# Performance work log

Measured on AMD Instinct MI355X. Metric: run time of the kernel, lower is better.

## Reference

```python
import jax, jax.numpy as jnp
import numpy as np

N_MESH, N_GRID, N_EDGES, D, H = 40962, 200000, 600000, 128, 128


def layer_norm(x, g, b, eps=1e-5):
    mu = x.mean(-1, keepdims=True)
    xc = x - mu
    var = (xc * xc).mean(-1, keepdims=True)
    return xc * jax.lax.rsqrt(var + eps) * g + b


def setup_inputs() -> dict:
    key = jax.random.key(0)
    ks = jax.random.split(key, 16)
    s = 1.0 / np.sqrt(D).astype(np.float32)
    s2 = 1.0 / np.sqrt(2 * D).astype(np.float32)
    return {
        "m2g_efeat": jax.random.normal(ks[0], (N_EDGES, D), jnp.float32),
        "grid_nfeat": jax.random.normal(ks[1], (N_GRID, D), jnp.float32),
        "mesh_nfeat": jax.random.normal(ks[2], (N_MESH, D), jnp.float32),
        "src_idx": jax.random.randint(ks[3], (N_EDGES,), 0, N_MESH, jnp.int32),
        "dst_idx": jnp.sort(jax.random.randint(ks[4], (N_EDGES,), 0, N_GRID, jnp.int32)),
        # edge TMLP (first linear split across efeat/src/dst -- equals Linear on concat)
        "We": jax.random.normal(ks[5], (D, H), jnp.float32) * s,
        "Ws": jax.random.normal(ks[6], (D, H), jnp.float32) * s,
        "Wd": jax.random.normal(ks[7], (D, H), jnp.float32) * s,
        "b0": jnp.zeros((H,), jnp.float32),
        "W1e": jax.random.normal(ks[8], (H, D), jnp.float32) * s,
        "b1e": jnp.zeros((D,), jnp.float32),
        "ge": jnp.ones((D,), jnp.float32),
        "be": jnp.zeros((D,), jnp.float32),
        # node MLP: input = concat(grid_nfeat, aggregated_efeat) -> 2D
        "Wn0": jax.random.normal(ks[9], (2 * D, H), jnp.float32) * s2,
        "bn0": jnp.zeros((H,), jnp.float32),
        "Wn1": jax.random.normal(ks[10], (H, D), jnp.float32) * s,
        "bn1": jnp.zeros((D,), jnp.float32),
        "gn": jnp.ones((D,), jnp.float32),
        "bn": jnp.zeros((D,), jnp.float32),
    }


def reference(m2g_efeat, grid_nfeat, mesh_nfeat, src_idx, dst_idx,
              We, Ws, Wd, b0, W1e, b1e, ge, be,
              Wn0, bn0, Wn1, bn1, gn, bn):
    # edge TMLP: project each input tensor then gather (CUGO truncated-MLP form)
    h = jax.nn.silu(m2g_efeat @ We
                    + (mesh_nfeat @ Ws)[src_idx]
                    + (grid_nfeat @ Wd)[dst_idx]
                    + b0)                                  # [E, H]
    efeat = layer_norm(h @ W1e + b1e, ge, be)              # [E, D]
    # sum aggregation edge->node, then concat with dst node features
    agg = jax.ops.segment_sum(efeat, dst_idx, num_segments=grid_nfeat.shape[0])  # [N_grid, D]
    cat = jnp.concatenate([grid_nfeat, agg], axis=-1)      # [N_grid, 2D]
    hn = jax.nn.silu(cat @ Wn0 + bn0)                      # [N_grid, H]
    dst = layer_norm(hn @ Wn1 + bn1, gn, bn) + grid_nfeat  # residual
    return dst
```

## Files before the change

### kernel.cpp

```cpp
#include <hip/hip_runtime.h>
#include <math.h>

#define NM 40962
#define NG 200000
#define NE 600000

typedef unsigned short u16;
typedef unsigned int u32;
typedef __attribute__((ext_vector_type(8))) short short8;
typedef __attribute__((ext_vector_type(4))) float f32x4;

#define OFF_WE 0
#define OFF_WS 16384
#define OFF_WD 32768
#define OFF_W1 49152
#define OFF_W0 65536
#define OFF_WN1 98304
__device__ u16 g_wp[114688];

__device__ __forceinline__ u32 f2bf(float f) {
  u32 u = __float_as_uint(f);
  return (u + 0x7FFFu + ((u >> 16) & 1u)) >> 16;
}
__device__ __forceinline__ float bfl(u32 h) { return __uint_as_float(h << 16); }
__device__ __forceinline__ float bsel(u32 w, int hiHalf) {
  return hiHalf ? __uint_as_float(w & 0xFFFF0000u) : __uint_as_float(w << 16);
}
__device__ __forceinline__ float silu_f(float x) { return x / (1.f + __expf(-x)); }

#define MFMA16(a, b, c) __builtin_amdgcn_mfma_f32_16x16x32_bf16(a, b, c, 0, 0, 0)

__device__ __forceinline__ void pk8(const float4& a, const float4& b, short8& hi,
                                    short8& lo) {
  float f[8] = {a.x, a.y, a.z, a.w, b.x, b.y, b.z, b.w};
#pragma unroll
  for (int j = 0; j < 8; ++j) {
    u32 h = f2bf(f[j]);
    hi[j] = (short)h;
    lo[j] = (short)f2bf(f[j] - bfl(h));
  }
}

__device__ __forceinline__ void afrag_hl(const float* __restrict__ X, int row, int k0,
                                         short8& hi, short8& lo) {
  const float4* p = (const float4*)(X + (size_t)row * 128 + k0);
  pk8(p[0], p[1], hi, lo);
}

template <int K>
__device__ __forceinline__ short8 bfrag(const u16* __restrict__ Wp, int n, int k0) {
  return *(const short8*)(Wp + (size_t)n * K + k0);
}

__global__ void prep_all(const float* __restrict__ We, const float* __restrict__ Ws,
                         const float* __restrict__ Wd, const float* __restrict__ W1e,
                         const float* __restrict__ Wn0, const float* __restrict__ Wn1) {
  for (int i = blockIdx.x * blockDim.x + threadIdx.x; i < 114688;
       i += gridDim.x * blockDim.x) {
    const float* W;
    int loc, kb;
    if (i < 16384)       { W = We;  loc = i;         kb = 7; }
    else if (i < 32768)  { W = Ws;  loc = i - 16384; kb = 7; }
    else if (i < 49152)  { W = Wd;  loc = i - 32768; kb = 7; }
    else if (i < 65536)  { W = W1e; loc = i - 49152; kb = 7; }
    else if (i < 98304)  { W = Wn0; loc = i - 65536; kb = 8; }
    else                 { W = Wn1; loc = i - 98304; kb = 7; }
    int n = loc >> kb, k = loc & ((1 << kb) - 1);
    g_wp[i] = (u16)f2bf(W[(size_t)k * 128 + n]);
  }
}

__global__ __launch_bounds__(256) void proj_kernel(const float* __restrict__ mesh,
                                                   const float* __restrict__ gridf,
                                                   uint4* __restrict__ PS,
                                                   uint4* __restrict__ PD,
                                                   float* __restrict__ agg) {
  const int TM = (NM + 31) / 32;
  const int TG = NG / 32;
  const int lane = threadIdx.x & 63, wv = threadIdx.x >> 6;
  const int g = lane >> 4, c = lane & 15;
  const int nw = gridDim.x * 4;
  for (int t = blockIdx.x * 4 + wv; t < TM + TG; t += nw) {
    const float* X;
    const u16* Wp;
    uint4* O;
    int n0, nrows, zero;
    if (t < TM) { X = mesh;  Wp = g_wp + OFF_WS; O = PS; n0 = t * 32;        nrows = NM; zero = 0; }
    else        { X = gridf; Wp = g_wp + OFF_WD; O = PD; n0 = (t - TM) * 32; nrows = NG; zero = 1; }
    f32x4 acc[2][8];
#pragma unroll
    for (int mt = 0; mt < 2; ++mt)
#pragma unroll
      for (int nt = 0; nt < 8; ++nt) {
        f32x4 z = {0.f, 0.f, 0.f, 0.f};
        acc[mt][nt] = z;
      }
#pragma unroll
    for (int kt = 0; kt < 4; ++kt) {
      short8 ah[2], al[2];
#pragma unroll
      for (int mt = 0; mt < 2; ++mt) {
        int row = n0 + 16 * mt + c;
        if (row >= nrows) row = nrows - 1;
        afrag_hl(X, row, 32 * kt + 8 * g, ah[mt], al[mt]);
      }
#pragma unroll
      for (int nt = 0; nt < 8; ++nt) {
        short8 b = bfrag<128>(Wp, 16 * nt + c, 32 * kt + 8 * g);
#pragma unroll
        for (int mt = 0; mt < 2; ++mt) {
          acc[mt][nt] = MFMA16(ah[mt], b, acc[mt][nt]);
          acc[mt][nt] = MFMA16(al[mt], b, acc[mt][nt]);
        }
      }
    }
#pragma unroll
    for (int mt = 0; mt < 2; ++mt)
#pragma unroll
      for (int r = 0; r < 4; ++r) {
        int row = n0 + 16 * mt + 4 * g + r;
        if (row < nrows) {
          uint4 v;
          v.x = f2bf(acc[mt][0][r]) | (f2bf(acc[mt][1][r]) << 16);
          v.y = f2bf(acc[mt][2][r]) | (f2bf(acc[mt][3][r]) << 16);
          v.z = f2bf(acc[mt][4][r]) | (f2bf(acc[mt][5][r]) << 16);
          v.w = f2bf(acc[mt][6][r]) | (f2bf(acc[mt][7][r]) << 16);
          O[(size_t)row * 16 + c] = v;
          if (zero) {
            float4 z = {0.f, 0.f, 0.f, 0.f};
            float4* ap = (float4*)(agg + (size_t)row * 128 + c * 8);
            ap[0] = z;
            ap[1] = z;
          }
        }
      }
  }
}

__global__ __launch_bounds__(256) void edge_kernel(
    const float* __restrict__ m2g, const uint4* __restrict__ PS,
    const uint4* __restrict__ PD, const int* __restrict__ src_idx,
    const int* __restrict__ dst_idx, const float* __restrict__ b0,
    const float* __restrict__ b1e, const float* __restrict__ ge,
    const float* __restrict__ be, float* __restrict__ agg) {
  const u16* WpE = g_wp + OFF_WE;
  const u16* Wp1 = g_wp + OFF_W1;
  __shared__ __align__(16) u16 hbh[4][32][128];
  __shared__ __align__(16) u16 hbl[4][32][128];
  const int lane = threadIdx.x & 63, wv = threadIdx.x >> 6;
  const int g = lane >> 4, c = lane & 15;
  float b0p[8];
#pragma unroll
  for (int nt = 0; nt < 8; ++nt) b0p[nt] = b0[16 * nt + c];
  const int nw = gridDim.x * 4;
  for (int t = blockIdx.x * 4 + wv; t < NE / 32; t += nw) {
    const int e0 = t * 32;
    float4 av[2][4][2];
#pragma unroll
    for (int mt = 0; mt < 2; ++mt)
#pragma unroll
      for (int kt = 0; kt < 4; ++kt) {
        const float4* p =
            (const float4*)(m2g + (size_t)(e0 + 16 * mt + c) * 128 + 32 * kt + 8 * g);
        av[mt][kt][0] = p[0];
        av[mt][kt][1] = p[1];
      }
    int dd[2][4];
    uint4 ps[2][4], pd[2][4];
#pragma unroll
    for (int mt = 0; mt < 2; ++mt)
#pragma unroll
      for (int r = 0; r < 4; ++r) {
        int e = e0 + 16 * mt + 4 * g + r;
        int s = src_idx[e];
        int d = dst_idx[e];
        dd[mt][r] = d;
        ps[mt][r] = PS[(size_t)s * 16 + c];
        pd[mt][r] = PD[(size_t)d * 16 + c];
      }
    f32x4 acc[2][8];
#pragma unroll
    for (int mt = 0; mt < 2; ++mt)
#pragma unroll
      for (int nt = 0; nt < 8; ++nt) {
        f32x4 z = {0.f, 0.f, 0.f, 0.f};
        acc[mt][nt] = z;
      }
#pragma unroll
    for (int kt = 0; kt < 4; ++kt) {
      short8 ah[2], al[2];
#pragma unroll
      for (int mt = 0; mt < 2; ++mt) pk8(av[mt][kt][0], av[mt][kt][1], ah[mt], al[mt]);
#pragma unroll
      for (int nt = 0; nt < 8; ++nt) {
        short8 b = bfrag<128>(WpE, 16 * nt + c, 32 * kt + 8 * g);
#pragma unroll
        for (int mt = 0; mt < 2; ++mt) {
          acc[mt][nt] = MFMA16(ah[mt], b, acc[mt][nt]);
          acc[mt][nt] = MFMA16(al[mt], b, acc[mt][nt]);
        }
      }
    }
#pragma unroll
    for (int mt = 0; mt < 2; ++mt)
#pragma unroll
      for (int nt = 0; nt < 8; ++nt)
#pragma unroll
        for (int r = 0; r < 4; ++r) {
          u32 pw = ((const u32*)&ps[mt][r])[nt >> 1];
          u32 qw = ((const u32*)&pd[mt][r])[nt >> 1];
          acc[mt][nt][r] += b0p[nt] + bsel(pw, nt & 1) + bsel(qw, nt & 1);
        }
#pragma unroll
    for (int mt = 0; mt < 2; ++mt)
#pragma unroll
      for (int r = 0; r < 4; ++r) {
        int row = 16 * mt + 4 * g + r;
        int sw = (row & 7) << 3;
#pragma unroll
        for (int nt = 0; nt < 8; ++nt) {
          float h = silu_f(acc[mt][nt][r]);
          u32 hb = f2bf(h);
          u32 lb = f2bf(h - bfl(hb));
          int idx = (16 * nt + c) ^ sw;
          hbh[wv][row][idx] = (u16)hb;
          hbl[wv][row][idx] = (u16)lb;
        }
      }
    f32x4 acc2[2][8];
    {
      float b1p[8];
#pragma unroll
      for (int nt = 0; nt < 8; ++nt) b1p[nt] = b1e[16 * nt + c];
#pragma unroll
      for (int mt = 0; mt < 2; ++mt)
#pragma unroll
        for (int nt = 0; nt < 8; ++nt) {
          f32x4 a = {b1p[nt], b1p[nt], b1p[nt], b1p[nt]};
          acc2[mt][nt] = a;
        }
    }
#pragma unroll
    for (int kt = 0; kt < 4; ++kt) {
      short8 ah[2], al[2];
#pragma unroll
      for (int mt = 0; mt < 2; ++mt) {
        int row = 16 * mt + c;
        int idx = (32 * kt + 8 * g) ^ ((c & 7) << 3);
        ah[mt] = *(const short8*)&hbh[wv][row][idx];
        al[mt] = *(const short8*)&hbl[wv][row][idx];
      }
#pragma unroll
      for (int nt = 0; nt < 8; ++nt) {
        short8 b = bfrag<128>(Wp1, 16 * nt + c, 32 * kt + 8 * g);
#pragma unroll
        for (int mt = 0; mt < 2; ++mt) {
          acc2[mt][nt] = MFMA16(ah[mt], b, acc2[mt][nt]);
          acc2[mt][nt] = MFMA16(al[mt], b, acc2[mt][nt]);
        }
      }
    }
    float gep[8], bep[8];
#pragma unroll
    for (int nt = 0; nt < 8; ++nt) {
      gep[nt] = ge[16 * nt + c];
      bep[nt] = be[16 * nt + c];
    }
#pragma unroll
    for (int mt = 0; mt < 2; ++mt) {
#pragma unroll
      for (int r = 0; r < 4; ++r) {
        float sm = 0.f, sq = 0.f;
#pragma unroll
        for (int nt = 0; nt < 8; ++nt) {
          float v = acc2[mt][nt][r];
          sm += v;
          sq += v * v;
        }
#pragma unroll
        for (int m = 1; m < 16; m <<= 1) {
          sm += __shfl_xor(sm, m, 64);
          sq += __shfl_xor(sq, m, 64);
        }
        float mu = sm * (1.f / 128.f);
        float var = sq * (1.f / 128.f) - mu * mu;
        float rs = rsqrtf(var + 1e-5f);
#pragma unroll
        for (int nt = 0; nt < 8; ++nt)
          acc2[mt][nt][r] = (acc2[mt][nt][r] - mu) * rs * gep[nt] + bep[nt];
      }
#pragma unroll
      for (int nt = 0; nt < 8; ++nt) {
        float a = acc2[mt][nt][0];
        int dp = dd[mt][0];
#pragma unroll
        for (int r = 1; r < 4; ++r) {
          if (dd[mt][r] == dp) {
            a += acc2[mt][nt][r];
          } else {
            atomicAdd(agg + (size_t)dp * 128 + 16 * nt + c, a);
            a = acc2[mt][nt][r];
            dp = dd[mt][r];
          }
        }
        atomicAdd(agg + (size_t)dp * 128 + 16 * nt + c, a);
      }
    }
  }
}

__global__ __launch_bounds__(256) void node_kernel(
    const float* __restrict__ gridf, const float* __restrict__ agg,
    const float* __restrict__ bn0, const float* __restrict__ bn1,
    const float* __restrict__ gn, const float* __restrict__ bnv,
    float* __restrict__ out) {
  const u16* Wp0 = g_wp + OFF_W0;
  const u16* Wp1 = g_wp + OFF_WN1;
  __shared__ __align__(16) u16 nbuf[4][32][128];
  const int lane = threadIdx.x & 63, wv = threadIdx.x >> 6;
  const int g = lane >> 4, c = lane & 15;
  float b0p[8], b1p[8];
#pragma unroll
  for (int nt = 0; nt < 8; ++nt) {
    b0p[nt] = bn0[16 * nt + c];
    b1p[nt] = bn1[16 * nt + c];
  }
  const int nw = gridDim.x * 4;
  for (int t = blockIdx.x * 4 + wv; t < NG / 32; t += nw) {
    const int n0 = t * 32;
    f32x4 acc[2][8];
#pragma unroll
    for (int mt = 0; mt < 2; ++mt)
#pragma unroll
      for (int nt = 0; nt < 8; ++nt) {
        f32x4 a = {b0p[nt], b0p[nt], b0p[nt], b0p[nt]};
        acc[mt][nt] = a;
      }
#pragma unroll
    for (int kt = 0; kt < 8; ++kt) {
      const float* src = (kt < 4) ? gridf : agg;
      int k0 = (kt & 3) * 32 + 8 * g;
      short8 ah[2], al[2];
#pragma unroll
      for (int mt = 0; mt < 2; ++mt) afrag_hl(src, n0 + 16 * mt + c, k0, ah[mt], al[mt]);
#pragma unroll
      for (int nt = 0; nt < 8; ++nt) {
        short8 b = bfrag<256>(Wp0, 16 * nt + c, 32 * kt + 8 * g);
#pragma unroll
        for (int mt = 0; mt < 2; ++mt) {
          acc[mt][nt] = MFMA16(ah[mt], b, acc[mt][nt]);
          acc[mt][nt] = MFMA16(al[mt], b, acc[mt][nt]);
        }
      }
    }
#pragma unroll
    for (int mt = 0; mt < 2; ++mt)
#pragma unroll
      for (int r = 0; r < 4; ++r) {
        int row = 16 * mt + 4 * g + r;
        int sw = (row & 7) << 3;
#pragma unroll
        for (int nt = 0; nt < 8; ++nt)
          nbuf[wv][row][(16 * nt + c) ^ sw] = (u16)f2bf(silu_f(acc[mt][nt][r]));
      }
    f32x4 acc2[2][8];
#pragma unroll
    for (int mt = 0; mt < 2; ++mt)
#pragma unroll
      for (int nt = 0; nt < 8; ++nt) {
        f32x4 a = {b1p[nt], b1p[nt], b1p[nt], b1p[nt]};
        acc2[mt][nt] = a;
      }
#pragma unroll
    for (int kt = 0; kt < 4; ++kt) {
      short8 ah[2];
#pragma unroll
      for (int mt = 0; mt < 2; ++mt) {
        int row = 16 * mt + c;
        ah[mt] = *(const short8*)&nbuf[wv][row][(32 * kt + 8 * g) ^ ((c & 7) << 3)];
      }
#pragma unroll
      for (int nt = 0; nt < 8; ++nt) {
        short8 b = bfrag<128>(Wp1, 16 * nt + c, 32 * kt + 8 * g);
#pragma unroll
        for (int mt = 0; mt < 2; ++mt) acc2[mt][nt] = MFMA16(ah[mt], b, acc2[mt][nt]);
      }
    }
    float gp[8], bp[8];
#pragma unroll
    for (int nt = 0; nt < 8; ++nt) {
      gp[nt] = gn[16 * nt + c];
      bp[nt] = bnv[16 * nt + c];
    }
#pragma unroll
    for (int mt = 0; mt < 2; ++mt)
#pragma unroll
      for (int r = 0; r < 4; ++r) {
        float sm = 0.f, sq = 0.f;
#pragma unroll
        for (int nt = 0; nt < 8; ++nt) {
          float v = acc2[mt][nt][r];
          sm += v;
          sq += v * v;
        }
#pragma unroll
        for (int m = 1; m < 16; m <<= 1) {
          sm += __shfl_xor(sm, m, 64);
          sq += __shfl_xor(sq, m, 64);
        }
        float mu = sm * (1.f / 128.f);
        float var = sq * (1.f / 128.f) - mu * mu;
        float rs = rsqrtf(var + 1e-5f);
        int row = n0 + 16 * mt + 4 * g + r;
#pragma unroll
        for (int nt = 0; nt < 8; ++nt) {
          size_t o = (size_t)row * 128 + 16 * nt + c;
          out[o] = (acc2[mt][nt][r] - mu) * rs * gp[nt] + bp[nt] + gridf[o];
        }
      }
  }
}

extern "C" void kernel_launch(void* const* d_in, const int* in_sizes, int n_in,
                              void* d_out, int out_size, void* d_ws, size_t ws_size,
                              hipStream_t stream) {
  const float* m2g = (const float*)d_in[0];
  const float* grid = (const float*)d_in[1];
  const float* mesh = (const float*)d_in[2];
  const int* src = (const int*)d_in[3];
  const int* dst = (const int*)d_in[4];
  const float* We = (const float*)d_in[5];
  const float* Ws = (const float*)d_in[6];
  const float* Wd = (const float*)d_in[7];
  const float* b0 = (const float*)d_in[8];
  const float* W1e = (const float*)d_in[9];
  const float* b1e = (const float*)d_in[10];
  const float* ge = (const float*)d_in[11];
  const float* be = (const float*)d_in[12];
  const float* Wn0 = (const float*)d_in[13];
  const float* bn0 = (const float*)d_in[14];
  const float* Wn1 = (const float*)d_in[15];
  const float* bn1 = (const float*)d_in[16];
  const float* gn = (const float*)d_in[17];
  const float* bnv = (const float*)d_in[18];
  (void)in_sizes; (void)n_in; (void)out_size; (void)ws_size;

  char* ws = (char*)d_ws;
  float* agg = (float*)ws;
  size_t aggB = (size_t)NG * 128 * 4;
  size_t psB = (size_t)NM * 256;
  uint4* PS = (uint4*)(ws + aggB);
  uint4* PD = (uint4*)(ws + aggB + psB);

  prep_all<<<224, 256, 0, stream>>>(We, Ws, Wd, W1e, Wn0, Wn1);
  proj_kernel<<<1024, 256, 0, stream>>>(mesh, grid, PS, PD, agg);
  edge_kernel<<<1536, 256, 0, stream>>>(m2g, PS, PD, src, dst, b0, b1e, ge, be, agg);
  node_kernel<<<1536, 256, 0, stream>>>(grid, agg, bn0, bn1, gn, bnv, (float*)d_out);
}
```

Baseline: 1.210 ms.

## Prefetch next tile's activations into registers across proj, edge and node kernels

Each persistent-wave loop now loads the A-operand rows for the next tile into registers right after the first GEMM's MFMAs, so the global loads overlap with the epilogue and second GEMM instead of stalling at the start of each iteration. The same software-pipelining pattern is applied to the projection, edge and node kernels. It costs extra VGPRs (64 in proj/edge, 128 floats in node), which may reduce occupancy or cause spills.

Measured after the change: 1.249 ms. 3.2% more time.

```diff
diff --git a/kernel.cpp b/kernel.cpp
--- a/kernel.cpp
+++ b/kernel.cpp
@@ -39,12 +39,6 @@
     hi[j] = (short)h;
     lo[j] = (short)f2bf(f[j] - bfl(h));
   }
-}
-
-__device__ __forceinline__ void afrag_hl(const float* __restrict__ X, int row, int k0,
-                                         short8& hi, short8& lo) {
-  const float4* p = (const float4*)(X + (size_t)row * 128 + k0);
-  pk8(p[0], p[1], hi, lo);
 }
 
 template <int K>
@@ -70,6 +64,13 @@
   }
 }
 
+__device__ __forceinline__ void proj_src(int t, const float* mesh, const float* gridf,
+                                         const float*& X, int& n0, int& nrows) {
+  const int TM = (NM + 31) / 32;
+  if (t < TM) { X = mesh;  n0 = t * 32;        nrows = NM; }
+  else        { X = gridf; n0 = (t - TM) * 32; nrows = NG; }
+}
+
 __global__ __launch_bounds__(256) void proj_kernel(const float* __restrict__ mesh,
                                                    const float* __restrict__ gridf,
                                                    uint4* __restrict__ PS,
@@ -77,16 +78,33 @@
                                                    float* __restrict__ agg) {
   const int TM = (NM + 31) / 32;
   const int TG = NG / 32;
+  const int T = TM + TG;
   const int lane = threadIdx.x & 63, wv = threadIdx.x >> 6;
   const int g = lane >> 4, c = lane & 15;
   const int nw = gridDim.x * 4;
-  for (int t = blockIdx.x * 4 + wv; t < TM + TG; t += nw) {
-    const float* X;
-    const u16* Wp;
-    uint4* O;
-    int n0, nrows, zero;
-    if (t < TM) { X = mesh;  Wp = g_wp + OFF_WS; O = PS; n0 = t * 32;        nrows = NM; zero = 0; }
-    else        { X = gridf; Wp = g_wp + OFF_WD; O = PD; n0 = (t - TM) * 32; nrows = NG; zero = 1; }
+  int t0 = blockIdx.x * 4 + wv;
+  if (t0 >= T) return;
+  float4 av[2][4][2];
+  {
+    const float* X; int n0, nrows;
+    proj_src(t0, mesh, gridf, X, n0, nrows);
+#pragma unroll
+    for (int mt = 0; mt < 2; ++mt)
+#pragma unroll
+      for (int kt = 0; kt < 4; ++kt) {
+        int row = n0 + 16 * mt + c;
+        if (row >= nrows) row = nrows - 1;
+        const float4* p = (const float4*)(X + (size_t)row * 128 + 32 * kt + 8 * g);
+        av[mt][kt][0] = p[0];
+        av[mt][kt][1] = p[1];
+      }
+  }
+  for (int t = t0; t < T; t += nw) {
+    const float* X; int n0, nrows;
+    proj_src(t, mesh, gridf, X, n0, nrows);
+    const u16* Wp = (t < TM) ? (g_wp + OFF_WS) : (g_wp + OFF_WD);
+    uint4* O = (t < TM) ? PS : PD;
+    int zero = (t >= TM);
     f32x4 acc[2][8];
 #pragma unroll
     for (int mt = 0; mt < 2; ++mt)
@@ -99,11 +117,7 @@
     for (int kt = 0; kt < 4; ++kt) {
       short8 ah[2], al[2];
 #pragma unroll
-      for (int mt = 0; mt < 2; ++mt) {
-        int row = n0 + 16 * mt + c;
-        if (row >= nrows) row = nrows - 1;
-        afrag_hl(X, row, 32 * kt + 8 * g, ah[mt], al[mt]);
-      }
+      for (int mt = 0; mt < 2; ++mt) pk8(av[mt][kt][0], av[mt][kt][1], ah[mt], al[mt]);
 #pragma unroll
       for (int nt = 0; nt < 8; ++nt) {
         short8 b = bfrag<128>(Wp, 16 * nt + c, 32 * kt + 8 * g);
@@ -112,6 +126,23 @@
           acc[mt][nt] = MFMA16(ah[mt], b, acc[mt][nt]);
           acc[mt][nt] = MFMA16(al[mt], b, acc[mt][nt]);
         }
+      }
+    }
+    {
+      int tn = t + nw;
+      if (tn < T) {
+        const float* Xn; int n0n, nrn;
+        proj_src(tn, mesh, gridf, Xn, n0n, nrn);
+#pragma unroll
+        for (int mt = 0; mt < 2; ++mt)
+#pragma unroll
+          for (int kt = 0; kt < 4; ++kt) {
+            int row = n0n + 16 * mt + c;
+            if (row >= nrn) row = nrn - 1;
+            const float4* p = (const float4*)(Xn + (size_t)row * 128 + 32 * kt + 8 * g);
+            av[mt][kt][0] = p[0];
+            av[mt][kt][1] = p[1];
+          }
       }
     }
 #pragma unroll
@@ -153,9 +184,12 @@
 #pragma unroll
   for (int nt = 0; nt < 8; ++nt) b0p[nt] = b0[16 * nt + c];
   const int nw = gridDim.x * 4;
-  for (int t = blockIdx.x * 4 + wv; t < NE / 32; t += nw) {
-    const int e0 = t * 32;
-    float4 av[2][4][2];
+  const int T = NE / 32;
+  int t0 = blockIdx.x * 4 + wv;
+  if (t0 >= T) return;
+  float4 av[2][4][2];
+  {
+    const int e0 = t0 * 32;
 #pragma unroll
     for (int mt = 0; mt < 2; ++mt)
 #pragma unroll
@@ -165,6 +199,9 @@
         av[mt][kt][0] = p[0];
         av[mt][kt][1] = p[1];
       }
+  }
+  for (int t = t0; t < T; t += nw) {
+    const int e0 = t * 32;
     int dd[2][4];
     uint4 ps[2][4], pd[2][4];
 #pragma unroll
@@ -199,6 +236,21 @@
           acc[mt][nt] = MFMA16(ah[mt], b, acc[mt][nt]);
           acc[mt][nt] = MFMA16(al[mt], b, acc[mt][nt]);
         }
+      }
+    }
+    {
+      int tn = t + nw;
+      if (tn < T) {
+        const int en = tn * 32;
+#pragma unroll
+        for (int mt = 0; mt < 2; ++mt)
+#pragma unroll
+          for (int kt = 0; kt < 4; ++kt) {
+            const float4* p =
+                (const float4*)(m2g + (size_t)(en + 16 * mt + c) * 128 + 32 * kt + 8 * g);
+            av[mt][kt][0] = p[0];
+            av[mt][kt][1] = p[1];
+          }
       }
     }
 #pragma unroll
@@ -326,7 +378,24 @@
     b1p[nt] = bn1[16 * nt + c];
   }
   const int nw = gridDim.x * 4;
-  for (int t = blockIdx.x * 4 + wv; t < NG / 32; t += nw) {
+  const int T = NG / 32;
+  int t0 = blockIdx.x * 4 + wv;
+  if (t0 >= T) return;
+  float4 av[2][8][2];
+  {
+    const int n0 = t0 * 32;
+#pragma unroll
+    for (int mt = 0; mt < 2; ++mt)
+#pragma unroll
+      for (int kt = 0; kt < 8; ++kt) {
+        const float* src = (kt < 4) ? gridf : agg;
+        const float4* p = (const float4*)(src + (size_t)(n0 + 16 * mt + c) * 128 +
+                                          (kt & 3) * 32 + 8 * g);
+        av[mt][kt][0] = p[0];
+        av[mt][kt][1] = p[1];
+      }
+  }
+  for (int t = t0; t < T; t += nw) {
     const int n0 = t * 32;
     f32x4 acc[2][8];
 #pragma unroll
@@ -338,11 +407,9 @@
       }
 #pragma unroll
     for (int kt = 0; kt < 8; ++kt) {
-      const float* src = (kt < 4) ? gridf : agg;
-      int k0 = (kt & 3) * 32 + 8 * g;
       short8 ah[2], al[2];
 #pragma unroll
-      for (int mt = 0; mt < 2; ++mt) afrag_hl(src, n0 + 16 * mt + c, k0, ah[mt], al[mt]);
+      for (int mt = 0; mt < 2; ++mt) pk8(av[mt][kt][0], av[mt][kt][1], ah[mt], al[mt]);
 #pragma unroll
       for (int nt = 0; nt < 8; ++nt) {
         short8 b = bfrag<256>(Wp0, 16 * nt + c, 32 * kt + 8 * g);
@@ -351,6 +418,22 @@
           acc[mt][nt] = MFMA16(ah[mt], b, acc[mt][nt]);
           acc[mt][nt] = MFMA16(al[mt], b, acc[mt][nt]);
         }
+      }
+    }
+    {
+      int tn = t + nw;
+      if (tn < T) {
+        const int n0n = tn * 32;
+#pragma unroll
+        for (int mt = 0; mt < 2; ++mt)
+#pragma unroll
+          for (int kt = 0; kt < 8; ++kt) {
+            const float* src = (kt < 4) ? gridf : agg;
+            const float4* p = (const float4*)(src + (size_t)(n0n + 16 * mt + c) * 128 +
+                                              (kt & 3) * 32 + 8 * g);
+            av[mt][kt][0] = p[0];
+            av[mt][kt][1] = p[1];
+          }
       }
     }
 #pragma unroll
```
